# Optimization experiments

Measured on AMD Instinct MI355X. Metric: run time of the kernel, lower is better.

Reference implementation:

```python
import jax, jax.numpy as jnp
import numpy as np

E = 128      # n_routed_experts (hardcoded in DS_CONFIG_FOR_NEMOTRON)
I = 1856     # moe_intermediate_size
K = 6        # num_experts_per_tok
H = 512      # config.hidden_size
T = 4096     # flattened tokens (batch*seq)
C = 320      # per-expert capacity; avg load = T*K/E = 192, C=320 makes drops ~impossible


def setup_inputs() -> dict:
    key = jax.random.key(0)
    k1, k2, k3, k4, k5 = jax.random.split(key, 5)
    return {
        "hidden_states": jax.random.normal(k1, (T, H), jnp.float32),
        "top_k_index": jax.random.randint(k2, (T, K), 0, E, jnp.int32),
        "top_k_weights": jax.random.uniform(k3, (T, K), jnp.float32),
        "w_gate_up": jax.random.normal(k4, (E, H, 2 * I), jnp.float32) * 0.02,
        "w_down": jax.random.normal(k5, (E, I, H), jnp.float32) * 0.02,
    }


def reference(hidden_states, top_k_index, top_k_weights, w_gate_up, w_down):
    # Grouped-GEMM formulation of the naive per-expert loop: sort the (token, k)
    # pairs by expert, pack each expert's tokens into a fixed-capacity buffer,
    # run batched gate/up/down GEMMs over all experts at once, then weighted
    # scatter-add back to token order. Same math as the torch loop.
    N = T * K
    e = top_k_index.reshape(N)                      # expert id per pair
    tok = jnp.repeat(jnp.arange(T), K)              # token id per pair
    w = top_k_weights.reshape(N)

    order = jnp.argsort(e)                          # stable sort by expert
    e_s, tok_s, w_s = e[order], tok[order], w[order]

    counts = jax.ops.segment_sum(jnp.ones((N,), jnp.int32), e, num_segments=E)
    starts = jnp.cumsum(counts) - counts            # exclusive prefix sum
    pos = jnp.arange(N) - starts[e_s]               # rank within expert
    valid = pos < C                                 # capacity guard (never trips at this load)
    slot = jnp.where(valid, e_s * C + pos, E * C)   # overflow -> dummy slot

    # Dispatch: [E*C+1, H] buffer of gathered token states (dummy row absorbs overflow)
    buf = jnp.zeros((E * C + 1, H), hidden_states.dtype).at[slot].set(hidden_states[tok_s])
    x = buf[: E * C].reshape(E, C, H)

    gu = jnp.einsum('ech,ehf->ecf', x, w_gate_up)   # [E, C, 2I]
    gate, up = jnp.split(gu, 2, axis=-1)
    inter = jax.nn.silu(gate) * up                  # [E, C, I]
    y = jnp.einsum('eci,eih->ech', inter, w_down).reshape(E * C, H)

    # Combine: gather each pair's expert output, scale by router weight, scatter-add by token
    gather_idx = jnp.where(valid, e_s * C + pos, 0)
    pair_y = y[gather_idx] * jnp.where(valid, w_s, 0.0)[:, None]
    out = jnp.zeros((T, H), hidden_states.dtype).at[tok_s].add(pair_y)
    # use_context_proj=False: context states alias the hidden states
    return (out, out)
```

## Files before the change

### kernel.cpp

```cpp
#include <hip/hip_runtime.h>
#include <hip/hip_bf16.h>
#include <stdint.h>

#define NE 128
#define NI 1856
#define NKK 6
#define NH 512
#define NT 4096
#define CAP 320
#define NPAIR (NT*NKK)
#define LD2I (2*NI)

typedef unsigned short u16;
typedef __attribute__((ext_vector_type(4))) float f32x4;
typedef __attribute__((ext_vector_type(8))) short bf16x8;
typedef __attribute__((ext_vector_type(4))) short s16x4;
typedef const void __attribute__((address_space(1)))* gas1p;
typedef void __attribute__((address_space(3)))* gas3p;

#define SFENCE __builtin_amdgcn_sched_barrier(0)

__device__ __forceinline__ short f2bf(float f) {
  union { __hip_bfloat16 h; short s; } c; c.h = __float2bfloat16(f); return c.s;
}
__device__ __forceinline__ float bf2f(short s) {
  union { float f; unsigned u; } v; v.u = ((unsigned)(u16)s) << 16; return v.f;
}

__device__ __forceinline__ int xcd_logical(int bid, int n) {
  int q = n >> 3, r = n & 7;
  int xcd = bid & 7, j = bid >> 3;
  return xcd * q + (xcd < r ? xcd : r) + j;
}

__global__ void k_route(const int* __restrict__ topk, int* __restrict__ counts,
                        int* __restrict__ slot_of_pair, int* __restrict__ pair_of_slot) {
  int n = blockIdx.x * 256 + threadIdx.x;
  if (n >= NPAIR) return;
  int e = topk[n];
  int p = atomicAdd(&counts[e], 1);
  int s = (p < CAP) ? e * CAP + p : -1;
  slot_of_pair[n] = s;
  if (s >= 0) pair_of_slot[s] = n;
}

__global__ void k_gather(const float* __restrict__ hid, const int* __restrict__ counts,
                         const int* __restrict__ pair_of_slot, u16* __restrict__ xbuf) {
  int t = threadIdx.x;
  int row = blockIdx.x * 2 + (t >> 7);
  int c = t & 127;
  int e = row / CAP, p = row % CAP;
  if (p >= counts[e]) return;
  int n = pair_of_slot[row];
  int tok = n / NKK;
  f32x4 v = *(const f32x4*)(hid + (size_t)tok * NH + c * 4);
  s16x4 o;
  o[0] = f2bf(v[0]); o[1] = f2bf(v[1]); o[2] = f2bf(v[2]); o[3] = f2bf(v[3]);
  *(s16x4*)(xbuf + (size_t)row * NH + c * 4) = o;
}

__global__ __launch_bounds__(256, 2) void k_gemm1(
    const u16* __restrict__ xbuf, const float* __restrict__ wgu,
    const int* __restrict__ counts, u16* __restrict__ inter, int e0, int nblk)
{
  __shared__ __align__(16) char lds[73728];
  int L = xcd_logical(blockIdx.x, nblk);
  int el = L / 58, nt = L % 58;
  int e = e0 + el;
  int cnt = counts[e]; if (cnt > CAP) cnt = CAP;
  int n0 = nt * 32;
  int t = threadIdx.x, w = t >> 6, l = t & 63;
  int wm = w >> 1, wc = w & 1;
  const char* abase = (const char*)(xbuf + (size_t)e * CAP * NH);

  int bks = l >> 4;
  int c4 = (l & 15) * 4;
  int gcol = (c4 < 32) ? (n0 + c4) : (NI + n0 + (c4 - 32));
  const float* bsrc = wgu + (size_t)e * NH * LD2I + gcol;

  int kg = l >> 4;
  int kg16 = kg * 16;
  int colg = wc * 16 + (l & 15);

  for (int base = 0; base < cnt; base += 256) {
    __syncthreads();

    auto STAGE = [&](int buf, int kt) {
      char* ad = lds + buf * 16384;
      #pragma unroll
      for (int i = 0; i < 4; ++i) {
        int seg = i * 4 + w;
        int o = seg * 1024 + l * 16;
        int r = o >> 6, slot = o & 63;
        int grow = base + r; if (grow > CAP - 1) grow = CAP - 1;
        const char* g = abase + (size_t)grow * (NH * 2) + kt * 64 + (slot ^ ((r & 3) << 4));
        __builtin_amdgcn_global_load_lds((gas1p)g, (gas3p)(ad + seg * 1024), 16, 0, 0);
      }
      char* bd = lds + 49152 + buf * 8192;
      #pragma unroll
      for (int i = 0; i < 2; ++i) {
        int seg = w * 2 + i;
        int k = seg * 4 + bks;
        const char* g = (const char*)(bsrc + (size_t)(kt * 32 + k) * LD2I);
        __builtin_amdgcn_global_load_lds((gas1p)g, (gas3p)(bd + seg * 1024), 16, 0, 0);
      }
    };

    f32x4 acc[2][4][2];
    #pragma unroll
    for (int m = 0; m < 2; ++m)
      #pragma unroll
      for (int f = 0; f < 4; ++f) { acc[m][f][0] = (f32x4){0,0,0,0}; acc[m][f][1] = (f32x4){0,0,0,0}; }

    STAGE(0, 0);
    STAGE(1, 1);
    SFENCE; asm volatile("s_waitcnt vmcnt(6) lgkmcnt(0)" ::: "memory"); SFENCE;

    for (int kt = 0; kt < 16; ++kt) {
      SFENCE; __builtin_amdgcn_s_barrier(); SFENCE;
      int sk = (kt + 2 < 16) ? kt + 2 : 15;
      STAGE((kt + 2) % 3, sk);

      const char* ab = lds + (kt % 3) * 16384;
      const char* bb = lds + 49152 + (kt % 3) * 8192;
      bf16x8 bg, bu;
      #pragma unroll
      for (int j = 0; j < 8; ++j) {
        int k = kg * 8 + j;
        bg[j] = f2bf(*(const float*)(bb + k * 256 + colg * 4));
        bu[j] = f2bf(*(const float*)(bb + k * 256 + (colg + 32) * 4));
      }
      #pragma unroll
      for (int mt = 0; mt < 2; ++mt)
        #pragma unroll
        for (int mf = 0; mf < 4; ++mf) {
          int r = mt * 128 + wm * 64 + mf * 16 + (l & 15);
          bf16x8 af = *(const bf16x8*)(ab + r * 64 + (kg16 ^ ((r & 3) << 4)));
          acc[mt][mf][0] = __builtin_amdgcn_mfma_f32_16x16x32_bf16(af, bg, acc[mt][mf][0], 0, 0, 0);
          acc[mt][mf][1] = __builtin_amdgcn_mfma_f32_16x16x32_bf16(af, bu, acc[mt][mf][1], 0, 0, 0);
        }
      SFENCE; asm volatile("s_waitcnt vmcnt(6) lgkmcnt(0)" ::: "memory"); SFENCE;
    }
    __syncthreads();

    int cl = wc * 16 + (l & 15);
    #pragma unroll
    for (int mt = 0; mt < 2; ++mt)
      #pragma unroll
      for (int mf = 0; mf < 4; ++mf) {
        f32x4 g = acc[mt][mf][0], u = acc[mt][mf][1];
        #pragma unroll
        for (int r = 0; r < 4; ++r) {
          float gv = g[r];
          float val = gv / (1.f + __expf(-gv)) * u[r];
          int rl = mt * 128 + wm * 64 + mf * 16 + (l >> 4) * 4 + r;
          *(short*)(lds + rl * 64 + ((cl * 2) ^ ((rl & 3) << 4))) = f2bf(val);
        }
      }
    __syncthreads();
    int rmax = cnt - base; if (rmax > 256) rmax = 256;
    u16* obase = inter + (size_t)(el * CAP + base) * NI + n0;
    #pragma unroll
    for (int i = 0; i < 4; ++i) {
      int task = i * 256 + t;
      int r = task >> 2, p = task & 3;
      if (r < rmax) {
        bf16x8 v = *(const bf16x8*)(lds + r * 64 + ((p * 16) ^ ((r & 3) << 4)));
        *(bf16x8*)(obase + (size_t)r * NI + p * 8) = v;
      }
    }
  }
}

__global__ __launch_bounds__(256, 2) void k_gemm2(
    const u16* __restrict__ inter, const float* __restrict__ wdn,
    const int* __restrict__ counts, u16* __restrict__ Y, int e0, int nblk)
{
  __shared__ __align__(16) char lds[73728];
  int L = xcd_logical(blockIdx.x, nblk);
  int el = L / 8, nt = L % 8;
  int e = e0 + el;
  int cnt = counts[e]; if (cnt > CAP) cnt = CAP;
  int n0 = nt * 64;
  int t = threadIdx.x, w = t >> 6, l = t & 63;
  int wm = w >> 1, wc = w & 1;
  const char* abase = (const char*)(inter + (size_t)el * CAP * NI);

  int bks = l >> 4;
  int c4 = (l & 15) * 4;
  const float* bsrc = wdn + (size_t)e * NI * NH + n0 + c4;

  int kg = l >> 4;
  int kg16 = kg * 16;
  int col0 = wc * 32 + (l & 15);

  for (int base = 0; base < cnt; base += 256) {
    __syncthreads();

    auto STAGE = [&](int buf, int kt) {
      char* ad = lds + buf * 16384;
      #pragma unroll
      for (int i = 0; i < 4; ++i) {
        int seg = i * 4 + w;
        int o = seg * 1024 + l * 16;
        int r = o >> 6, slot = o & 63;
        int grow = base + r; if (grow > CAP - 1) grow = CAP - 1;
        const char* g = abase + (size_t)grow * (NI * 2) + kt * 64 + (slot ^ ((r & 3) << 4));
        __builtin_amdgcn_global_load_lds((gas1p)g, (gas3p)(ad + seg * 1024), 16, 0, 0);
      }
      char* bd = lds + 49152 + buf * 8192;
      #pragma unroll
      for (int i = 0; i < 2; ++i) {
        int seg = w * 2 + i;
        int k = seg * 4 + bks;
        const char* g = (const char*)(bsrc + (size_t)(kt * 32 + k) * NH);
        __builtin_amdgcn_global_load_lds((gas1p)g, (gas3p)(bd + seg * 1024), 16, 0, 0);
      }
    };

    f32x4 acc[2][4][2];
    #pragma unroll
    for (int m = 0; m < 2; ++m)
      #pragma unroll
      for (int f = 0; f < 4; ++f) { acc[m][f][0] = (f32x4){0,0,0,0}; acc[m][f][1] = (f32x4){0,0,0,0}; }

    STAGE(0, 0);
    STAGE(1, 1);
    SFENCE; asm volatile("s_waitcnt vmcnt(6) lgkmcnt(0)" ::: "memory"); SFENCE;

    for (int kt = 0; kt < 58; ++kt) {
      SFENCE; __builtin_amdgcn_s_barrier(); SFENCE;
      int sk = (kt + 2 < 58) ? kt + 2 : 57;
      STAGE((kt + 2) % 3, sk);

      const char* ab = lds + (kt % 3) * 16384;
      const char* bb = lds + 49152 + (kt % 3) * 8192;
      bf16x8 b0, b1;
      #pragma unroll
      for (int j = 0; j < 8; ++j) {
        int k = kg * 8 + j;
        b0[j] = f2bf(*(const float*)(bb + k * 256 + col0 * 4));
        b1[j] = f2bf(*(const float*)(bb + k * 256 + (col0 + 16) * 4));
      }
      #pragma unroll
      for (int mt = 0; mt < 2; ++mt)
        #pragma unroll
        for (int mf = 0; mf < 4; ++mf) {
          int r = mt * 128 + wm * 64 + mf * 16 + (l & 15);
          bf16x8 af = *(const bf16x8*)(ab + r * 64 + (kg16 ^ ((r & 3) << 4)));
          acc[mt][mf][0] = __builtin_amdgcn_mfma_f32_16x16x32_bf16(af, b0, acc[mt][mf][0], 0, 0, 0);
          acc[mt][mf][1] = __builtin_amdgcn_mfma_f32_16x16x32_bf16(af, b1, acc[mt][mf][1], 0, 0, 0);
        }
      SFENCE; asm volatile("s_waitcnt vmcnt(6) lgkmcnt(0)" ::: "memory"); SFENCE;
    }
    __syncthreads();

    #pragma unroll
    for (int mt = 0; mt < 2; ++mt)
      #pragma unroll
      for (int mf = 0; mf < 4; ++mf)
        #pragma unroll
        for (int f = 0; f < 2; ++f) {
          f32x4 a = acc[mt][mf][f];
          int cl = wc * 32 + f * 16 + (l & 15);
          #pragma unroll
          for (int r = 0; r < 4; ++r) {
            int rl = mt * 128 + wm * 64 + mf * 16 + (l >> 4) * 4 + r;
            *(short*)(lds + rl * 128 + ((cl * 2) ^ ((rl & 7) << 4))) = f2bf(a[r]);
          }
        }
    __syncthreads();
    int rmax = cnt - base; if (rmax > 256) rmax = 256;
    u16* obase = Y + (size_t)(e * CAP + base) * NH + n0;
    #pragma unroll
    for (int i = 0; i < 8; ++i) {
      int task = i * 256 + t;
      int r = task >> 3, p = task & 7;
      if (r < rmax) {
        bf16x8 v = *(const bf16x8*)(lds + r * 128 + ((p * 16) ^ ((r & 7) << 4)));
        *(bf16x8*)(obase + (size_t)r * NH + p * 8) = v;
      }
    }
  }
}

__global__ void k_combine(const int* __restrict__ slot_of_pair, const float* __restrict__ wts,
                          const u16* __restrict__ Y, float* __restrict__ out)
{
  int t = threadIdx.x;
  int tok = blockIdx.x * 2 + (t >> 7);
  int c = t & 127;
  f32x4 a = (f32x4){0.f, 0.f, 0.f, 0.f};
  #pragma unroll
  for (int k = 0; k < NKK; ++k) {
    int n = tok * NKK + k;
    int s = slot_of_pair[n];
    if (s >= 0) {
      float wv = wts[n];
      s16x4 y = *(const s16x4*)(Y + (size_t)s * NH + c * 4);
      a[0] += wv * bf2f(y[0]);
      a[1] += wv * bf2f(y[1]);
      a[2] += wv * bf2f(y[2]);
      a[3] += wv * bf2f(y[3]);
    }
  }
  *(f32x4*)(out + (size_t)tok * NH + c * 4) = a;
  *(f32x4*)(out + (size_t)(NT + tok) * NH + c * 4) = a;
}

extern "C" void kernel_launch(void* const* d_in, const int* in_sizes, int n_in,
                              void* d_out, int out_size, void* d_ws, size_t ws_size,
                              hipStream_t stream) {
  const float* hid  = (const float*)d_in[0];
  const int*   topk = (const int*)d_in[1];
  const float* wts  = (const float*)d_in[2];
  const float* wgu  = (const float*)d_in[3];
  const float* wdn  = (const float*)d_in[4];

  char* ws = (char*)d_ws;
  size_t off = 0;
  auto alloc = [&](size_t sz) { char* p = ws + off; off = (off + sz + 255) & ~(size_t)255; return p; };
  int* counts        = (int*)alloc(NE * 4);
  int* slot_of_pair  = (int*)alloc((size_t)NPAIR * 4);
  int* pair_of_slot  = (int*)alloc((size_t)NE * CAP * 4);
  u16* xbuf          = (u16*)alloc((size_t)NE * CAP * NH * 2);
  u16* Y             = (u16*)alloc((size_t)NE * CAP * NH * 2);
  size_t remain = ws_size > off ? ws_size - off : 0;
  size_t per_e = (size_t)CAP * NI * 2;
  int chunkE = (int)(remain / per_e);
  if (chunkE > NE) chunkE = NE;
  if (chunkE < 1) chunkE = 1;
  u16* inter = (u16*)(ws + off);

  hipMemsetAsync(counts, 0, NE * 4, stream);
  k_route<<<NPAIR / 256, 256, 0, stream>>>(topk, counts, slot_of_pair, pair_of_slot);
  k_gather<<<NE * CAP / 2, 256, 0, stream>>>(hid, counts, pair_of_slot, xbuf);
  for (int e0 = 0; e0 < NE; e0 += chunkE) {
    int ce = NE - e0 < chunkE ? NE - e0 : chunkE;
    int nb1 = ce * 58;
    int nb2 = ce * 8;
    k_gemm1<<<nb1, 256, 0, stream>>>(xbuf, wgu, counts, inter, e0, nb1);
    k_gemm2<<<nb2, 256, 0, stream>>>(inter, wdn, counts, Y, e0, nb2);
  }
  k_combine<<<NT / 2, 256, 0, stream>>>(slot_of_pair, wts, Y, (float*)d_out);
}
```

Measured before the change: 534.5 us.

## Load fp32 weights directly to registers and double-buffer A tiles in LDS

Both GEMM kernels stop staging the fp32 weight tile through LDS. Each lane now loads its own B values straight from global memory into a ping-pong register array, and the A tile pipeline goes from triple to double buffering. LDS use drops from 72KB to 32KB per block, so launch bounds rise to three blocks per CU for more occupancy. The risks are uncoalesced strided global loads for B (one float per lane per row), more register pressure from the two 16-float arrays, and a shallower prefetch depth. The epilogue still reuses LDS, which fits within 32KB.

```diff
diff --git a/kernel.cpp b/kernel.cpp
--- a/kernel.cpp
+++ b/kernel.cpp
@@ -59,11 +59,55 @@
   *(s16x4*)(xbuf + (size_t)row * NH + c * 4) = o;
 }
 
-__global__ __launch_bounds__(256, 2) void k_gemm1(
+#define G1_STAGE_A(BUF, KT_) do { \
+    char* ad_ = lds + (BUF) * 16384; \
+    _Pragma("unroll") \
+    for (int i_ = 0; i_ < 4; ++i_) { \
+      int seg_ = i_ * 4 + w; \
+      int o_ = seg_ * 1024 + l * 16; \
+      int r_ = o_ >> 6, slot_ = o_ & 63; \
+      int grow_ = base + r_; if (grow_ > CAP - 1) grow_ = CAP - 1; \
+      const char* g_ = abase + (size_t)grow_ * (NH * 2) + (size_t)(KT_) * 64 + (slot_ ^ ((r_ & 3) << 4)); \
+      __builtin_amdgcn_global_load_lds((gas1p)g_, (gas3p)(ad_ + seg_ * 1024), 16, 0, 0); \
+    } } while (0)
+
+#define G1_LOAD_B(DST, KT_) do { \
+    const float* pg_ = bsrcg + (size_t)((KT_) * 32 + kg * 8) * LD2I; \
+    _Pragma("unroll") \
+    for (int j_ = 0; j_ < 8; ++j_) { \
+      DST[j_]     = pg_[(size_t)j_ * LD2I]; \
+      DST[8 + j_] = pg_[(size_t)j_ * LD2I + NI]; \
+    } } while (0)
+
+#define G1_COMPUTE(P, CUR) do { \
+    const char* ab_ = lds + (P) * 16384; \
+    bf16x8 bg_, bu_; \
+    _Pragma("unroll") \
+    for (int j_ = 0; j_ < 8; ++j_) { bg_[j_] = f2bf(CUR[j_]); bu_[j_] = f2bf(CUR[8 + j_]); } \
+    _Pragma("unroll") \
+    for (int mt_ = 0; mt_ < 2; ++mt_) \
+      _Pragma("unroll") \
+      for (int mf_ = 0; mf_ < 4; ++mf_) { \
+        int r_ = mt_ * 128 + wm * 64 + mf_ * 16 + (l & 15); \
+        bf16x8 af_ = *(const bf16x8*)(ab_ + r_ * 64 + (kg16 ^ ((r_ & 3) << 4))); \
+        acc[mt_][mf_][0] = __builtin_amdgcn_mfma_f32_16x16x32_bf16(af_, bg_, acc[mt_][mf_][0], 0, 0, 0); \
+        acc[mt_][mf_][1] = __builtin_amdgcn_mfma_f32_16x16x32_bf16(af_, bu_, acc[mt_][mf_][1], 0, 0, 0); \
+      } } while (0)
+
+#define G1_ITER(X, CUR, NXT, BUFC) do { \
+    SFENCE; __builtin_amdgcn_s_barrier(); SFENCE; \
+    { int nk_ = (X) + 1 < 16 ? (X) + 1 : 15; \
+      G1_STAGE_A((BUFC) ^ 1, nk_); SFENCE; G1_LOAD_B(NXT, nk_); } \
+    SFENCE; \
+    G1_COMPUTE(BUFC, CUR); \
+    SFENCE; asm volatile("s_waitcnt vmcnt(16)" ::: "memory"); SFENCE; \
+  } while (0)
+
+__global__ __launch_bounds__(256, 3) void k_gemm1(
     const u16* __restrict__ xbuf, const float* __restrict__ wgu,
     const int* __restrict__ counts, u16* __restrict__ inter, int e0, int nblk)
 {
-  __shared__ __align__(16) char lds[73728];
+  __shared__ __align__(16) char lds[32768];
   int L = xcd_logical(blockIdx.x, nblk);
   int el = L / 58, nt = L % 58;
   int e = e0 + el;
@@ -73,73 +117,29 @@
   int wm = w >> 1, wc = w & 1;
   const char* abase = (const char*)(xbuf + (size_t)e * CAP * NH);
 
-  int bks = l >> 4;
-  int c4 = (l & 15) * 4;
-  int gcol = (c4 < 32) ? (n0 + c4) : (NI + n0 + (c4 - 32));
-  const float* bsrc = wgu + (size_t)e * NH * LD2I + gcol;
-
   int kg = l >> 4;
   int kg16 = kg * 16;
   int colg = wc * 16 + (l & 15);
+  const float* bsrcg = wgu + (size_t)e * NH * LD2I + n0 + colg;
+
+  float bva[16], bvb[16];
 
   for (int base = 0; base < cnt; base += 256) {
     __syncthreads();
-
-    auto STAGE = [&](int buf, int kt) {
-      char* ad = lds + buf * 16384;
-      #pragma unroll
-      for (int i = 0; i < 4; ++i) {
-        int seg = i * 4 + w;
-        int o = seg * 1024 + l * 16;
-        int r = o >> 6, slot = o & 63;
-        int grow = base + r; if (grow > CAP - 1) grow = CAP - 1;
-        const char* g = abase + (size_t)grow * (NH * 2) + kt * 64 + (slot ^ ((r & 3) << 4));
-        __builtin_amdgcn_global_load_lds((gas1p)g, (gas3p)(ad + seg * 1024), 16, 0, 0);
-      }
-      char* bd = lds + 49152 + buf * 8192;
-      #pragma unroll
-      for (int i = 0; i < 2; ++i) {
-        int seg = w * 2 + i;
-        int k = seg * 4 + bks;
-        const char* g = (const char*)(bsrc + (size_t)(kt * 32 + k) * LD2I);
-        __builtin_amdgcn_global_load_lds((gas1p)g, (gas3p)(bd + seg * 1024), 16, 0, 0);
-      }
-    };
-
     f32x4 acc[2][4][2];
     #pragma unroll
     for (int m = 0; m < 2; ++m)
       #pragma unroll
       for (int f = 0; f < 4; ++f) { acc[m][f][0] = (f32x4){0,0,0,0}; acc[m][f][1] = (f32x4){0,0,0,0}; }
 
-    STAGE(0, 0);
-    STAGE(1, 1);
-    SFENCE; asm volatile("s_waitcnt vmcnt(6) lgkmcnt(0)" ::: "memory"); SFENCE;
-
-    for (int kt = 0; kt < 16; ++kt) {
-      SFENCE; __builtin_amdgcn_s_barrier(); SFENCE;
-      int sk = (kt + 2 < 16) ? kt + 2 : 15;
-      STAGE((kt + 2) % 3, sk);
-
-      const char* ab = lds + (kt % 3) * 16384;
-      const char* bb = lds + 49152 + (kt % 3) * 8192;
-      bf16x8 bg, bu;
-      #pragma unroll
-      for (int j = 0; j < 8; ++j) {
-        int k = kg * 8 + j;
-        bg[j] = f2bf(*(const float*)(bb + k * 256 + colg * 4));
-        bu[j] = f2bf(*(const float*)(bb + k * 256 + (colg + 32) * 4));
-      }
-      #pragma unroll
-      for (int mt = 0; mt < 2; ++mt)
-        #pragma unroll
-        for (int mf = 0; mf < 4; ++mf) {
-          int r = mt * 128 + wm * 64 + mf * 16 + (l & 15);
-          bf16x8 af = *(const bf16x8*)(ab + r * 64 + (kg16 ^ ((r & 3) << 4)));
-          acc[mt][mf][0] = __builtin_amdgcn_mfma_f32_16x16x32_bf16(af, bg, acc[mt][mf][0], 0, 0, 0);
-          acc[mt][mf][1] = __builtin_amdgcn_mfma_f32_16x16x32_bf16(af, bu, acc[mt][mf][1], 0, 0, 0);
-        }
-      SFENCE; asm volatile("s_waitcnt vmcnt(6) lgkmcnt(0)" ::: "memory"); SFENCE;
+    G1_STAGE_A(0, 0);
+    SFENCE;
+    G1_LOAD_B(bva, 0);
+    SFENCE; asm volatile("s_waitcnt vmcnt(16)" ::: "memory"); SFENCE;
+
+    for (int kt = 0; kt < 16; kt += 2) {
+      G1_ITER(kt,     bva, bvb, 0);
+      G1_ITER(kt + 1, bvb, bva, 1);
     }
     __syncthreads();
 
@@ -172,11 +172,55 @@
   }
 }
 
-__global__ __launch_bounds__(256, 2) void k_gemm2(
+#define G2_STAGE_A(BUF, KT_) do { \
+    char* ad_ = lds + (BUF) * 16384; \
+    _Pragma("unroll") \
+    for (int i_ = 0; i_ < 4; ++i_) { \
+      int seg_ = i_ * 4 + w; \
+      int o_ = seg_ * 1024 + l * 16; \
+      int r_ = o_ >> 6, slot_ = o_ & 63; \
+      int grow_ = base + r_; if (grow_ > CAP - 1) grow_ = CAP - 1; \
+      const char* g_ = abase + (size_t)grow_ * (NI * 2) + (size_t)(KT_) * 64 + (slot_ ^ ((r_ & 3) << 4)); \
+      __builtin_amdgcn_global_load_lds((gas1p)g_, (gas3p)(ad_ + seg_ * 1024), 16, 0, 0); \
+    } } while (0)
+
+#define G2_LOAD_B(DST, KT_) do { \
+    const float* pd_ = bsrcd + (size_t)((KT_) * 32 + kg * 8) * NH; \
+    _Pragma("unroll") \
+    for (int j_ = 0; j_ < 8; ++j_) { \
+      DST[j_]     = pd_[(size_t)j_ * NH]; \
+      DST[8 + j_] = pd_[(size_t)j_ * NH + 16]; \
+    } } while (0)
+
+#define G2_COMPUTE(P, CUR) do { \
+    const char* ab_ = lds + (P) * 16384; \
+    bf16x8 b0_, b1_; \
+    _Pragma("unroll") \
+    for (int j_ = 0; j_ < 8; ++j_) { b0_[j_] = f2bf(CUR[j_]); b1_[j_] = f2bf(CUR[8 + j_]); } \
+    _Pragma("unroll") \
+    for (int mt_ = 0; mt_ < 2; ++mt_) \
+      _Pragma("unroll") \
+      for (int mf_ = 0; mf_ < 4; ++mf_) { \
+        int r_ = mt_ * 128 + wm * 64 + mf_ * 16 + (l & 15); \
+        bf16x8 af_ = *(const bf16x8*)(ab_ + r_ * 64 + (kg16 ^ ((r_ & 3) << 4))); \
+        acc[mt_][mf_][0] = __builtin_amdgcn_mfma_f32_16x16x32_bf16(af_, b0_, acc[mt_][mf_][0], 0, 0, 0); \
+        acc[mt_][mf_][1] = __builtin_amdgcn_mfma_f32_16x16x32_bf16(af_, b1_, acc[mt_][mf_][1], 0, 0, 0); \
+      } } while (0)
+
+#define G2_ITER(X, CUR, NXT, BUFC) do { \
+    SFENCE; __builtin_amdgcn_s_barrier(); SFENCE; \
+    { int nk_ = (X) + 1 < 58 ? (X) + 1 : 57; \
+      G2_STAGE_A((BUFC) ^ 1, nk_); SFENCE; G2_LOAD_B(NXT, nk_); } \
+    SFENCE; \
+    G2_COMPUTE(BUFC, CUR); \
+    SFENCE; asm volatile("s_waitcnt vmcnt(16)" ::: "memory"); SFENCE; \
+  } while (0)
+
+__global__ __launch_bounds__(256, 3) void k_gemm2(
     const u16* __restrict__ inter, const float* __restrict__ wdn,
     const int* __restrict__ counts, u16* __restrict__ Y, int e0, int nblk)
 {
-  __shared__ __align__(16) char lds[73728];
+  __shared__ __align__(16) char lds[32768];
   int L = xcd_logical(blockIdx.x, nblk);
   int el = L / 8, nt = L % 8;
   int e = e0 + el;
@@ -186,72 +230,29 @@
   int wm = w >> 1, wc = w & 1;
   const char* abase = (const char*)(inter + (size_t)el * CAP * NI);
 
-  int bks = l >> 4;
-  int c4 = (l & 15) * 4;
-  const float* bsrc = wdn + (size_t)e * NI * NH + n0 + c4;
-
   int kg = l >> 4;
   int kg16 = kg * 16;
   int col0 = wc * 32 + (l & 15);
+  const float* bsrcd = wdn + (size_t)e * NI * NH + n0 + col0;
+
+  float bva[16], bvb[16];
 
   for (int base = 0; base < cnt; base += 256) {
     __syncthreads();
-
-    auto STAGE = [&](int buf, int kt) {
-      char* ad = lds + buf * 16384;
-      #pragma unroll
-      for (int i = 0; i < 4; ++i) {
-        int seg = i * 4 + w;
-        int o = seg * 1024 + l * 16;
-        int r = o >> 6, slot = o & 63;
-        int grow = base + r; if (grow > CAP - 1) grow = CAP - 1;
-        const char* g = abase + (size_t)grow * (NI * 2) + kt * 64 + (slot ^ ((r & 3) << 4));
-        __builtin_amdgcn_global_load_lds((gas1p)g, (gas3p)(ad + seg * 1024), 16, 0, 0);
-      }
-      char* bd = lds + 49152 + buf * 8192;
-      #pragma unroll
-      for (int i = 0; i < 2; ++i) {
-        int seg = w * 2 + i;
-        int k = seg * 4 + bks;
-        const char* g = (const char*)(bsrc + (size_t)(kt * 32 + k) * NH);
-        __builtin_amdgcn_global_load_lds((gas1p)g, (gas3p)(bd + seg * 1024), 16, 0, 0);
-      }
-    };
-
     f32x4 acc[2][4][2];
     #pragma unroll
     for (int m = 0; m < 2; ++m)
       #pragma unroll
       for (int f = 0; f < 4; ++f) { acc[m][f][0] = (f32x4){0,0,0,0}; acc[m][f][1] = (f32x4){0,0,0,0}; }
 
-    STAGE(0, 0);
-    STAGE(1, 1);
-    SFENCE; asm volatile("s_waitcnt vmcnt(6) lgkmcnt(0)" ::: "memory"); SFENCE;
-
-    for (int kt = 0; kt < 58; ++kt) {
-      SFENCE; __builtin_amdgcn_s_barrier(); SFENCE;
-      int sk = (kt + 2 < 58) ? kt + 2 : 57;
-      STAGE((kt + 2) % 3, sk);
-
-      const char* ab = lds + (kt % 3) * 16384;
-      const char* bb = lds + 49152 + (kt % 3) * 8192;
-      bf16x8 b0, b1;
-      #pragma unroll
-      for (int j = 0; j < 8; ++j) {
-        int k = kg * 8 + j;
-        b0[j] = f2bf(*(const float*)(bb + k * 256 + col0 * 4));
-        b1[j] = f2bf(*(const float*)(bb + k * 256 + (col0 + 16) * 4));
-      }
-      #pragma unroll
-      for (int mt = 0; mt < 2; ++mt)
-        #pragma unroll
-        for (int mf = 0; mf < 4; ++mf) {
-          int r = mt * 128 + wm * 64 + mf * 16 + (l & 15);
-          bf16x8 af = *(const bf16x8*)(ab + r * 64 + (kg16 ^ ((r & 3) << 4)));
-          acc[mt][mf][0] = __builtin_amdgcn_mfma_f32_16x16x32_bf16(af, b0, acc[mt][mf][0], 0, 0, 0);
-          acc[mt][mf][1] = __builtin_amdgcn_mfma_f32_16x16x32_bf16(af, b1, acc[mt][mf][1], 0, 0, 0);
-        }
-      SFENCE; asm volatile("s_waitcnt vmcnt(6) lgkmcnt(0)" ::: "memory"); SFENCE;
+    G2_STAGE_A(0, 0);
+    SFENCE;
+    G2_LOAD_B(bva, 0);
+    SFENCE; asm volatile("s_waitcnt vmcnt(16)" ::: "memory"); SFENCE;
+
+    for (int kt = 0; kt < 58; kt += 2) {
+      G2_ITER(kt,     bva, bvb, 0);
+      G2_ITER(kt + 1, bvb, bva, 1);
     }
     __syncthreads();
 
```

Measured after the change: 739.0 us. 1.38x slower.

## Restructure gate/up GEMM to keep A rows in registers and sweep all N tiles

Applied to the files above, without the earlier changes.

k_gemm1 now launches 3 blocks per expert, each covering 128 token rows. Each block holds its A fragments (bf16 activations) entirely in registers and loops over all 58 output column tiles, streaming fp32 weights through registers into a double-buffered, transposed bf16 LDS tile. Before, each of 58 blocks per expert reloaded the full activation tile from global memory, so this removes that redundant A traffic and the fp32-to-bf16 conversion on the LDS read side. The cost is far fewer blocks (about 384 instead of 7424), 512 threads per block and high register pressure from 32 bf16x8 A fragments, which risks low occupancy and poor CU utilisation on a large GPU.

```diff
diff --git a/kernel.cpp b/kernel.cpp
--- a/kernel.cpp
+++ b/kernel.cpp
@@ -19,6 +19,8 @@
 typedef void __attribute__((address_space(3)))* gas3p;
 
 #define SFENCE __builtin_amdgcn_sched_barrier(0)
+#define BARLDS() do { SFENCE; asm volatile("s_waitcnt lgkmcnt(0)" ::: "memory"); SFENCE; \
+                      __builtin_amdgcn_s_barrier(); SFENCE; } while (0)
 
 __device__ __forceinline__ short f2bf(float f) {
   union { __hip_bfloat16 h; short s; } c; c.h = __float2bfloat16(f); return c.s;
@@ -59,114 +61,103 @@
   *(s16x4*)(xbuf + (size_t)row * NH + c * 4) = o;
 }
 
-__global__ __launch_bounds__(256, 2) void k_gemm1(
+__global__ __launch_bounds__(512, 2) void k_gemm1(
     const u16* __restrict__ xbuf, const float* __restrict__ wgu,
     const int* __restrict__ counts, u16* __restrict__ inter, int e0, int nblk)
 {
-  __shared__ __align__(16) char lds[73728];
+  __shared__ __align__(256) char lds[18432];
   int L = xcd_logical(blockIdx.x, nblk);
-  int el = L / 58, nt = L % 58;
+  int el = L / 3, mt = L % 3;
   int e = e0 + el;
   int cnt = counts[e]; if (cnt > CAP) cnt = CAP;
-  int n0 = nt * 32;
+  int row0 = mt * 128;
+  if (row0 >= cnt) return;
   int t = threadIdx.x, w = t >> 6, l = t & 63;
-  int wm = w >> 1, wc = w & 1;
-  const char* abase = (const char*)(xbuf + (size_t)e * CAP * NH);
-
-  int bks = l >> 4;
-  int c4 = (l & 15) * 4;
-  int gcol = (c4 < 32) ? (n0 + c4) : (NI + n0 + (c4 - 32));
-  const float* bsrc = wgu + (size_t)e * NH * LD2I + gcol;
-
-  int kg = l >> 4;
-  int kg16 = kg * 16;
-  int colg = wc * 16 + (l & 15);
-
-  for (int base = 0; base < cnt; base += 256) {
-    __syncthreads();
-
-    auto STAGE = [&](int buf, int kt) {
-      char* ad = lds + buf * 16384;
-      #pragma unroll
-      for (int i = 0; i < 4; ++i) {
-        int seg = i * 4 + w;
-        int o = seg * 1024 + l * 16;
-        int r = o >> 6, slot = o & 63;
-        int grow = base + r; if (grow > CAP - 1) grow = CAP - 1;
-        const char* g = abase + (size_t)grow * (NH * 2) + kt * 64 + (slot ^ ((r & 3) << 4));
-        __builtin_amdgcn_global_load_lds((gas1p)g, (gas3p)(ad + seg * 1024), 16, 0, 0);
-      }
-      char* bd = lds + 49152 + buf * 8192;
-      #pragma unroll
-      for (int i = 0; i < 2; ++i) {
-        int seg = w * 2 + i;
-        int k = seg * 4 + bks;
-        const char* g = (const char*)(bsrc + (size_t)(kt * 32 + k) * LD2I);
-        __builtin_amdgcn_global_load_lds((gas1p)g, (gas3p)(bd + seg * 1024), 16, 0, 0);
-      }
-    };
-
-    f32x4 acc[2][4][2];
-    #pragma unroll
-    for (int m = 0; m < 2; ++m)
-      #pragma unroll
-      for (int f = 0; f < 4; ++f) { acc[m][f][0] = (f32x4){0,0,0,0}; acc[m][f][1] = (f32x4){0,0,0,0}; }
-
-    STAGE(0, 0);
-    STAGE(1, 1);
-    SFENCE; asm volatile("s_waitcnt vmcnt(6) lgkmcnt(0)" ::: "memory"); SFENCE;
-
+  int wm = w >> 1, wn = w & 1;
+  int kg = l >> 4, kg16 = kg * 16;
+  int krow = w * 4 + kg;
+  int c0 = (l & 15) * 4;
+  int gc = (c0 < 32) ? c0 : (NI - 32 + c0);
+  const float* bsrc = wgu + (size_t)e * NH * LD2I + gc + (size_t)krow * LD2I;
+  int colg = wn * 16 + (l & 15);
+  int cxor = (colg & 6) << 3;
+
+  bf16x8 a0[16], a1[16];
+  {
+    int r0 = row0 + wm * 32 + (l & 15);
+    int ra = r0     > CAP - 1 ? CAP - 1 : r0;
+    int rb = r0 + 16 > CAP - 1 ? CAP - 1 : r0 + 16;
+    const char* apa = (const char*)(xbuf + ((size_t)e * CAP + ra) * NH) + kg16;
+    const char* apb = (const char*)(xbuf + ((size_t)e * CAP + rb) * NH) + kg16;
+    #pragma unroll
     for (int kt = 0; kt < 16; ++kt) {
-      SFENCE; __builtin_amdgcn_s_barrier(); SFENCE;
-      int sk = (kt + 2 < 16) ? kt + 2 : 15;
-      STAGE((kt + 2) % 3, sk);
-
-      const char* ab = lds + (kt % 3) * 16384;
-      const char* bb = lds + 49152 + (kt % 3) * 8192;
-      bf16x8 bg, bu;
-      #pragma unroll
-      for (int j = 0; j < 8; ++j) {
-        int k = kg * 8 + j;
-        bg[j] = f2bf(*(const float*)(bb + k * 256 + colg * 4));
-        bu[j] = f2bf(*(const float*)(bb + k * 256 + (colg + 32) * 4));
-      }
-      #pragma unroll
-      for (int mt = 0; mt < 2; ++mt)
-        #pragma unroll
-        for (int mf = 0; mf < 4; ++mf) {
-          int r = mt * 128 + wm * 64 + mf * 16 + (l & 15);
-          bf16x8 af = *(const bf16x8*)(ab + r * 64 + (kg16 ^ ((r & 3) << 4)));
-          acc[mt][mf][0] = __builtin_amdgcn_mfma_f32_16x16x32_bf16(af, bg, acc[mt][mf][0], 0, 0, 0);
-          acc[mt][mf][1] = __builtin_amdgcn_mfma_f32_16x16x32_bf16(af, bu, acc[mt][mf][1], 0, 0, 0);
-        }
-      SFENCE; asm volatile("s_waitcnt vmcnt(6) lgkmcnt(0)" ::: "memory"); SFENCE;
-    }
-    __syncthreads();
-
-    int cl = wc * 16 + (l & 15);
-    #pragma unroll
-    for (int mt = 0; mt < 2; ++mt)
-      #pragma unroll
-      for (int mf = 0; mf < 4; ++mf) {
-        f32x4 g = acc[mt][mf][0], u = acc[mt][mf][1];
-        #pragma unroll
-        for (int r = 0; r < 4; ++r) {
-          float gv = g[r];
-          float val = gv / (1.f + __expf(-gv)) * u[r];
-          int rl = mt * 128 + wm * 64 + mf * 16 + (l >> 4) * 4 + r;
-          *(short*)(lds + rl * 64 + ((cl * 2) ^ ((rl & 3) << 4))) = f2bf(val);
-        }
-      }
-    __syncthreads();
-    int rmax = cnt - base; if (rmax > 256) rmax = 256;
-    u16* obase = inter + (size_t)(el * CAP + base) * NI + n0;
-    #pragma unroll
-    for (int i = 0; i < 4; ++i) {
-      int task = i * 256 + t;
-      int r = task >> 2, p = task & 3;
+      a0[kt] = *(const bf16x8*)(apa + kt * 64);
+      a1[kt] = *(const bf16x8*)(apb + kt * 64);
+    }
+  }
+
+  auto LB = [&](int f) -> f32x4 {
+    int nt2 = f >> 4, kt2 = f & 15;
+    if (nt2 > 57) { nt2 = 57; kt2 = 15; }
+    return *(const f32x4*)(bsrc + (size_t)kt2 * 32 * LD2I + nt2 * 32);
+  };
+  auto WB = [&](char* bb, f32x4 v) {
+    #pragma unroll
+    for (int j = 0; j < 4; ++j) {
+      int col = c0 + j;
+      *(short*)(bb + col * 80 + ((krow * 2) ^ ((col & 6) << 3))) = f2bf(v[j]);
+    }
+  };
+
+  f32x4 rb[4];
+  rb[0] = LB(0); rb[1] = LB(1); rb[2] = LB(2);
+  WB(lds, rb[0]);
+
+  char* rp = lds + 10240;
+  for (int nt = 0; nt < 58; ++nt) {
+    int n0 = nt * 32;
+    int ii0 = nt * 16;
+    f32x4 ag[2], au[2];
+    ag[0] = (f32x4){0,0,0,0}; ag[1] = (f32x4){0,0,0,0};
+    au[0] = (f32x4){0,0,0,0}; au[1] = (f32x4){0,0,0,0};
+
+    #pragma unroll
+    for (int kt = 0; kt < 16; ++kt) {
+      BARLDS();
+      rb[(kt + 3) & 3] = LB(ii0 + kt + 3);
+      SFENCE;
+      char* bb1 = lds + (((kt + 1) & 1) * 5120);
+      WB(bb1, rb[(kt + 1) & 3]);
+      const char* bb0 = lds + ((kt & 1) * 5120);
+      bf16x8 bg = *(const bf16x8*)(bb0 + colg * 80 + (kg16 ^ cxor));
+      bf16x8 bu = *(const bf16x8*)(bb0 + (32 + colg) * 80 + (kg16 ^ cxor));
+      ag[0] = __builtin_amdgcn_mfma_f32_16x16x32_bf16(a0[kt], bg, ag[0], 0, 0, 0);
+      au[0] = __builtin_amdgcn_mfma_f32_16x16x32_bf16(a0[kt], bu, au[0], 0, 0, 0);
+      ag[1] = __builtin_amdgcn_mfma_f32_16x16x32_bf16(a1[kt], bg, ag[1], 0, 0, 0);
+      au[1] = __builtin_amdgcn_mfma_f32_16x16x32_bf16(a1[kt], bu, au[1], 0, 0, 0);
+    }
+
+    BARLDS();
+    #pragma unroll
+    for (int mf = 0; mf < 2; ++mf) {
+      f32x4 g = (mf == 0) ? ag[0] : ag[1];
+      f32x4 u = (mf == 0) ? au[0] : au[1];
+      #pragma unroll
+      for (int r = 0; r < 4; ++r) {
+        float gv = g[r];
+        float val = gv / (1.f + __expf(-gv)) * u[r];
+        int rl = wm * 32 + mf * 16 + kg * 4 + r;
+        int cl = wn * 16 + (l & 15);
+        *(short*)(rp + rl * 64 + ((cl * 2) ^ ((rl & 3) << 4))) = f2bf(val);
+      }
+    }
+    BARLDS();
+    int rmax = cnt - row0; if (rmax > 128) rmax = 128;
+    {
+      int r = t >> 2, p = t & 3;
       if (r < rmax) {
-        bf16x8 v = *(const bf16x8*)(lds + r * 64 + ((p * 16) ^ ((r & 3) << 4)));
-        *(bf16x8*)(obase + (size_t)r * NI + p * 8) = v;
+        bf16x8 v = *(const bf16x8*)(rp + r * 64 + ((p * 16) ^ ((r & 3) << 4)));
+        *(bf16x8*)(inter + ((size_t)(el * CAP + row0 + r)) * NI + n0 + p * 8) = v;
       }
     }
   }
@@ -337,9 +328,9 @@
   k_gather<<<NE * CAP / 2, 256, 0, stream>>>(hid, counts, pair_of_slot, xbuf);
   for (int e0 = 0; e0 < NE; e0 += chunkE) {
     int ce = NE - e0 < chunkE ? NE - e0 : chunkE;
-    int nb1 = ce * 58;
+    int nb1 = ce * 3;
     int nb2 = ce * 8;
-    k_gemm1<<<nb1, 256, 0, stream>>>(xbuf, wgu, counts, inter, e0, nb1);
+    k_gemm1<<<nb1, 512, 0, stream>>>(xbuf, wgu, counts, inter, e0, nb1);
     k_gemm2<<<nb2, 256, 0, stream>>>(inter, wdn, counts, Y, e0, nb2);
   }
   k_combine<<<NT / 2, 256, 0, stream>>>(slot_of_pair, wts, Y, (float*)d_out);
```

Result: slower. 947.4 us (+77.3%).

## Double N-tile width in both expert GEMMs and double-buffer A separately

Applied to the files above, without the earlier changes.

Widens the N tile of the gate/up GEMM from 32 to 64 columns and of the down GEMM from 64 to 128 columns, halving the grid and the number of times each expert's A rows are reloaded. The A tile moves to a 2-deep buffer while the B (fp32 weight) tile stays 3-deep, with the wait counts adjusted for the new load counts. Each wave now holds twice as many accumulators, which raises register pressure and LDS use (80 KB per block) and may hurt occupancy. With half as many blocks the grid is smaller, which can leave the machine less evenly loaded.

```diff
diff --git a/kernel.cpp b/kernel.cpp
--- a/kernel.cpp
+++ b/kernel.cpp
@@ -63,29 +63,27 @@
     const u16* __restrict__ xbuf, const float* __restrict__ wgu,
     const int* __restrict__ counts, u16* __restrict__ inter, int e0, int nblk)
 {
-  __shared__ __align__(16) char lds[73728];
+  __shared__ __align__(16) char lds[81920];
   int L = xcd_logical(blockIdx.x, nblk);
-  int el = L / 58, nt = L % 58;
+  int el = L / 29, nt = L % 29;
   int e = e0 + el;
   int cnt = counts[e]; if (cnt > CAP) cnt = CAP;
-  int n0 = nt * 32;
+  int n0 = nt * 64;
   int t = threadIdx.x, w = t >> 6, l = t & 63;
   int wm = w >> 1, wc = w & 1;
   const char* abase = (const char*)(xbuf + (size_t)e * CAP * NH);
 
-  int bks = l >> 4;
-  int c4 = (l & 15) * 4;
-  int gcol = (c4 < 32) ? (n0 + c4) : (NI + n0 + (c4 - 32));
-  const float* bsrc = wgu + (size_t)e * NH * LD2I + gcol;
-
-  int kg = l >> 4;
-  int kg16 = kg * 16;
-  int colg = wc * 16 + (l & 15);
+  int ch = l & 31;
+  int gc = (ch < 16) ? (n0 + ch * 4) : (NI + n0 + (ch - 16) * 4);
+  const float* bsrc0 = wgu + (size_t)e * NH * LD2I + gc + (size_t)(l >> 5) * LD2I;
+
+  int kg = l >> 4, kg16 = kg * 16;
+  int colg = wc * 32 + (l & 15);
 
   for (int base = 0; base < cnt; base += 256) {
     __syncthreads();
 
-    auto STAGE = [&](int buf, int kt) {
+    auto STAGE_A = [&](int buf, int kt) {
       char* ad = lds + buf * 16384;
       #pragma unroll
       for (int i = 0; i < 4; ++i) {
@@ -96,76 +94,90 @@
         const char* g = abase + (size_t)grow * (NH * 2) + kt * 64 + (slot ^ ((r & 3) << 4));
         __builtin_amdgcn_global_load_lds((gas1p)g, (gas3p)(ad + seg * 1024), 16, 0, 0);
       }
-      char* bd = lds + 49152 + buf * 8192;
-      #pragma unroll
-      for (int i = 0; i < 2; ++i) {
-        int seg = w * 2 + i;
-        int k = seg * 4 + bks;
-        const char* g = (const char*)(bsrc + (size_t)(kt * 32 + k) * LD2I);
+    };
+    auto STAGE_B = [&](int buf, int kt) {
+      char* bd = lds + 32768 + buf * 16384;
+      #pragma unroll
+      for (int i = 0; i < 4; ++i) {
+        int seg = w * 4 + i;
+        const char* g = (const char*)(bsrc0 + (size_t)(kt * 32 + seg * 2) * LD2I);
         __builtin_amdgcn_global_load_lds((gas1p)g, (gas3p)(bd + seg * 1024), 16, 0, 0);
       }
     };
 
-    f32x4 acc[2][4][2];
+    f32x4 ag[2][4][2], au[2][4][2];
     #pragma unroll
     for (int m = 0; m < 2; ++m)
       #pragma unroll
-      for (int f = 0; f < 4; ++f) { acc[m][f][0] = (f32x4){0,0,0,0}; acc[m][f][1] = (f32x4){0,0,0,0}; }
-
-    STAGE(0, 0);
-    STAGE(1, 1);
-    SFENCE; asm volatile("s_waitcnt vmcnt(6) lgkmcnt(0)" ::: "memory"); SFENCE;
+      for (int f = 0; f < 4; ++f)
+        #pragma unroll
+        for (int n = 0; n < 2; ++n) { ag[m][f][n] = (f32x4){0,0,0,0}; au[m][f][n] = (f32x4){0,0,0,0}; }
+
+    STAGE_A(0, 0);
+    STAGE_B(0, 0);
+    STAGE_B(1, 1);
+    SFENCE; asm volatile("s_waitcnt vmcnt(4) lgkmcnt(0)" ::: "memory"); SFENCE;
 
     for (int kt = 0; kt < 16; ++kt) {
       SFENCE; __builtin_amdgcn_s_barrier(); SFENCE;
+      int ak = (kt + 1 < 16) ? kt + 1 : 15;
       int sk = (kt + 2 < 16) ? kt + 2 : 15;
-      STAGE((kt + 2) % 3, sk);
-
-      const char* ab = lds + (kt % 3) * 16384;
-      const char* bb = lds + 49152 + (kt % 3) * 8192;
-      bf16x8 bg, bu;
-      #pragma unroll
-      for (int j = 0; j < 8; ++j) {
-        int k = kg * 8 + j;
-        bg[j] = f2bf(*(const float*)(bb + k * 256 + colg * 4));
-        bu[j] = f2bf(*(const float*)(bb + k * 256 + (colg + 32) * 4));
-      }
+      STAGE_A((kt + 1) & 1, ak);
+      STAGE_B((kt + 2) % 3, sk);
+
+      const char* ab = lds + (kt & 1) * 16384;
+      const char* bb = lds + 32768 + (kt % 3) * 16384;
+      bf16x8 bg[2], bu[2];
+      #pragma unroll
+      for (int nf = 0; nf < 2; ++nf)
+        #pragma unroll
+        for (int j = 0; j < 8; ++j) {
+          int k = kg * 8 + j;
+          int c = colg + nf * 16;
+          bg[nf][j] = f2bf(*(const float*)(bb + k * 512 + c * 4));
+          bu[nf][j] = f2bf(*(const float*)(bb + k * 512 + 256 + c * 4));
+        }
       #pragma unroll
       for (int mt = 0; mt < 2; ++mt)
         #pragma unroll
         for (int mf = 0; mf < 4; ++mf) {
           int r = mt * 128 + wm * 64 + mf * 16 + (l & 15);
           bf16x8 af = *(const bf16x8*)(ab + r * 64 + (kg16 ^ ((r & 3) << 4)));
-          acc[mt][mf][0] = __builtin_amdgcn_mfma_f32_16x16x32_bf16(af, bg, acc[mt][mf][0], 0, 0, 0);
-          acc[mt][mf][1] = __builtin_amdgcn_mfma_f32_16x16x32_bf16(af, bu, acc[mt][mf][1], 0, 0, 0);
-        }
-      SFENCE; asm volatile("s_waitcnt vmcnt(6) lgkmcnt(0)" ::: "memory"); SFENCE;
-    }
-    __syncthreads();
-
-    int cl = wc * 16 + (l & 15);
+          #pragma unroll
+          for (int nf = 0; nf < 2; ++nf) {
+            ag[mt][mf][nf] = __builtin_amdgcn_mfma_f32_16x16x32_bf16(af, bg[nf], ag[mt][mf][nf], 0, 0, 0);
+            au[mt][mf][nf] = __builtin_amdgcn_mfma_f32_16x16x32_bf16(af, bu[nf], au[mt][mf][nf], 0, 0, 0);
+          }
+        }
+      SFENCE; asm volatile("s_waitcnt vmcnt(4) lgkmcnt(0)" ::: "memory"); SFENCE;
+    }
+    __syncthreads();
+
     #pragma unroll
     for (int mt = 0; mt < 2; ++mt)
       #pragma unroll
-      for (int mf = 0; mf < 4; ++mf) {
-        f32x4 g = acc[mt][mf][0], u = acc[mt][mf][1];
-        #pragma unroll
-        for (int r = 0; r < 4; ++r) {
-          float gv = g[r];
-          float val = gv / (1.f + __expf(-gv)) * u[r];
-          int rl = mt * 128 + wm * 64 + mf * 16 + (l >> 4) * 4 + r;
-          *(short*)(lds + rl * 64 + ((cl * 2) ^ ((rl & 3) << 4))) = f2bf(val);
-        }
-      }
+      for (int mf = 0; mf < 4; ++mf)
+        #pragma unroll
+        for (int nf = 0; nf < 2; ++nf) {
+          f32x4 g = ag[mt][mf][nf], u = au[mt][mf][nf];
+          int cl = wc * 32 + nf * 16 + (l & 15);
+          #pragma unroll
+          for (int r = 0; r < 4; ++r) {
+            float gv = g[r];
+            float val = gv / (1.f + __expf(-gv)) * u[r];
+            int rl = mt * 128 + wm * 64 + mf * 16 + (l >> 4) * 4 + r;
+            *(short*)(lds + rl * 128 + ((cl * 2) ^ ((rl & 7) << 4))) = f2bf(val);
+          }
+        }
     __syncthreads();
     int rmax = cnt - base; if (rmax > 256) rmax = 256;
     u16* obase = inter + (size_t)(el * CAP + base) * NI + n0;
     #pragma unroll
-    for (int i = 0; i < 4; ++i) {
+    for (int i = 0; i < 8; ++i) {
       int task = i * 256 + t;
-      int r = task >> 2, p = task & 3;
+      int r = task >> 3, p = task & 7;
       if (r < rmax) {
-        bf16x8 v = *(const bf16x8*)(lds + r * 64 + ((p * 16) ^ ((r & 3) << 4)));
+        bf16x8 v = *(const bf16x8*)(lds + r * 128 + ((p * 16) ^ ((r & 7) << 4)));
         *(bf16x8*)(obase + (size_t)r * NI + p * 8) = v;
       }
     }
@@ -176,28 +188,26 @@
     const u16* __restrict__ inter, const float* __restrict__ wdn,
     const int* __restrict__ counts, u16* __restrict__ Y, int e0, int nblk)
 {
-  __shared__ __align__(16) char lds[73728];
+  __shared__ __align__(16) char lds[81920];
   int L = xcd_logical(blockIdx.x, nblk);
-  int el = L / 8, nt = L % 8;
+  int el = L / 4, nt = L % 4;
   int e = e0 + el;
   int cnt = counts[e]; if (cnt > CAP) cnt = CAP;
-  int n0 = nt * 64;
+  int n0 = nt * 128;
   int t = threadIdx.x, w = t >> 6, l = t & 63;
   int wm = w >> 1, wc = w & 1;
   const char* abase = (const char*)(inter + (size_t)el * CAP * NI);
 
-  int bks = l >> 4;
-  int c4 = (l & 15) * 4;
-  const float* bsrc = wdn + (size_t)e * NI * NH + n0 + c4;
-
-  int kg = l >> 4;
-  int kg16 = kg * 16;
-  int col0 = wc * 32 + (l & 15);
+  int ch = l & 31;
+  const float* bsrc0 = wdn + (size_t)e * NI * NH + n0 + ch * 4 + (size_t)(l >> 5) * NH;
+
+  int kg = l >> 4, kg16 = kg * 16;
+  int col0 = wc * 64 + (l & 15);
 
   for (int base = 0; base < cnt; base += 256) {
     __syncthreads();
 
-    auto STAGE = [&](int buf, int kt) {
+    auto STAGE_A = [&](int buf, int kt) {
       char* ad = lds + buf * 16384;
       #pragma unroll
       for (int i = 0; i < 4; ++i) {
@@ -208,50 +218,58 @@
         const char* g = abase + (size_t)grow * (NI * 2) + kt * 64 + (slot ^ ((r & 3) << 4));
         __builtin_amdgcn_global_load_lds((gas1p)g, (gas3p)(ad + seg * 1024), 16, 0, 0);
       }
-      char* bd = lds + 49152 + buf * 8192;
-      #pragma unroll
-      for (int i = 0; i < 2; ++i) {
-        int seg = w * 2 + i;
-        int k = seg * 4 + bks;
-        const char* g = (const char*)(bsrc + (size_t)(kt * 32 + k) * NH);
+    };
+    auto STAGE_B = [&](int buf, int kt) {
+      char* bd = lds + 32768 + buf * 16384;
+      #pragma unroll
+      for (int i = 0; i < 4; ++i) {
+        int seg = w * 4 + i;
+        const char* g = (const char*)(bsrc0 + (size_t)(kt * 32 + seg * 2) * NH);
         __builtin_amdgcn_global_load_lds((gas1p)g, (gas3p)(bd + seg * 1024), 16, 0, 0);
       }
     };
 
-    f32x4 acc[2][4][2];
+    f32x4 acc[2][4][4];
     #pragma unroll
     for (int m = 0; m < 2; ++m)
       #pragma unroll
-      for (int f = 0; f < 4; ++f) { acc[m][f][0] = (f32x4){0,0,0,0}; acc[m][f][1] = (f32x4){0,0,0,0}; }
-
-    STAGE(0, 0);
-    STAGE(1, 1);
-    SFENCE; asm volatile("s_waitcnt vmcnt(6) lgkmcnt(0)" ::: "memory"); SFENCE;
+      for (int f = 0; f < 4; ++f)
+        #pragma unroll
+        for (int n = 0; n < 4; ++n) acc[m][f][n] = (f32x4){0,0,0,0};
+
+    STAGE_A(0, 0);
+    STAGE_B(0, 0);
+    STAGE_B(1, 1);
+    SFENCE; asm volatile("s_waitcnt vmcnt(4) lgkmcnt(0)" ::: "memory"); SFENCE;
 
     for (int kt = 0; kt < 58; ++kt) {
       SFENCE; __builtin_amdgcn_s_barrier(); SFENCE;
+      int ak = (kt + 1 < 58) ? kt + 1 : 57;
       int sk = (kt + 2 < 58) ? kt + 2 : 57;
-      STAGE((kt + 2) % 3, sk);
-
-      const char* ab = lds + (kt % 3) * 16384;
-      const char* bb = lds + 49152 + (kt % 3) * 8192;
-      bf16x8 b0, b1;
-      #pragma unroll
-      for (int j = 0; j < 8; ++j) {
-        int k = kg * 8 + j;
-        b0[j] = f2bf(*(const float*)(bb + k * 256 + col0 * 4));
-        b1[j] = f2bf(*(const float*)(bb + k * 256 + (col0 + 16) * 4));
-      }
+      STAGE_A((kt + 1) & 1, ak);
+      STAGE_B((kt + 2) % 3, sk);
+
+      const char* ab = lds + (kt & 1) * 16384;
+      const char* bb = lds + 32768 + (kt % 3) * 16384;
+      bf16x8 bf[4];
+      #pragma unroll
+      for (int nf = 0; nf < 4; ++nf)
+        #pragma unroll
+        for (int j = 0; j < 8; ++j) {
+          int k = kg * 8 + j;
+          bf[nf][j] = f2bf(*(const float*)(bb + k * 512 + (col0 + nf * 16) * 4));
+        }
       #pragma unroll
       for (int mt = 0; mt < 2; ++mt)
         #pragma unroll
         for (int mf = 0; mf < 4; ++mf) {
           int r = mt * 128 + wm * 64 + mf * 16 + (l & 15);
           bf16x8 af = *(const bf16x8*)(ab + r * 64 + (kg16 ^ ((r & 3) << 4)));
-          acc[mt][mf][0] = __builtin_amdgcn_mfma_f32_16x16x32_bf16(af, b0, acc[mt][mf][0], 0, 0, 0);
-          acc[mt][mf][1] = __builtin_amdgcn_mfma_f32_16x16x32_bf16(af, b1, acc[mt][mf][1], 0, 0, 0);
-        }
-      SFENCE; asm volatile("s_waitcnt vmcnt(6) lgkmcnt(0)" ::: "memory"); SFENCE;
+          #pragma unroll
+          for (int nf = 0; nf < 4; ++nf)
+            acc[mt][mf][nf] = __builtin_amdgcn_mfma_f32_16x16x32_bf16(af, bf[nf], acc[mt][mf][nf], 0, 0, 0);
+        }
+      SFENCE; asm volatile("s_waitcnt vmcnt(4) lgkmcnt(0)" ::: "memory"); SFENCE;
     }
     __syncthreads();
 
@@ -260,24 +278,24 @@
       #pragma unroll
       for (int mf = 0; mf < 4; ++mf)
         #pragma unroll
-        for (int f = 0; f < 2; ++f) {
-          f32x4 a = acc[mt][mf][f];
-          int cl = wc * 32 + f * 16 + (l & 15);
+        for (int nf = 0; nf < 4; ++nf) {
+          f32x4 a = acc[mt][mf][nf];
+          int cl = wc * 64 + nf * 16 + (l & 15);
           #pragma unroll
           for (int r = 0; r < 4; ++r) {
             int rl = mt * 128 + wm * 64 + mf * 16 + (l >> 4) * 4 + r;
-            *(short*)(lds + rl * 128 + ((cl * 2) ^ ((rl & 7) << 4))) = f2bf(a[r]);
+            *(short*)(lds + rl * 256 + ((cl * 2) ^ ((rl & 7) << 4))) = f2bf(a[r]);
           }
         }
     __syncthreads();
     int rmax = cnt - base; if (rmax > 256) rmax = 256;
     u16* obase = Y + (size_t)(e * CAP + base) * NH + n0;
     #pragma unroll
-    for (int i = 0; i < 8; ++i) {
+    for (int i = 0; i < 16; ++i) {
       int task = i * 256 + t;
-      int r = task >> 3, p = task & 7;
+      int r = task >> 4, p = task & 15;
       if (r < rmax) {
-        bf16x8 v = *(const bf16x8*)(lds + r * 128 + ((p * 16) ^ ((r & 7) << 4)));
+        bf16x8 v = *(const bf16x8*)(lds + r * 256 + ((p * 16) ^ ((r & 7) << 4)));
         *(bf16x8*)(obase + (size_t)r * NH + p * 8) = v;
       }
     }
@@ -337,8 +355,8 @@
   k_gather<<<NE * CAP / 2, 256, 0, stream>>>(hid, counts, pair_of_slot, xbuf);
   for (int e0 = 0; e0 < NE; e0 += chunkE) {
     int ce = NE - e0 < chunkE ? NE - e0 : chunkE;
-    int nb1 = ce * 58;
-    int nb2 = ce * 8;
+    int nb1 = ce * 29;
+    int nb2 = ce * 4;
     k_gemm1<<<nb1, 256, 0, stream>>>(xbuf, wgu, counts, inter, e0, nb1);
     k_gemm2<<<nb2, 256, 0, stream>>>(inter, wdn, counts, Y, e0, nb2);
   }
```

Measured after the change: 678.1 us. 26.9% more time.
